# Optimization experiments

Measured on AMD Instinct MI355X. Metric: run time of the kernel, lower is better.

The kernel has to match this reference:

```python
import jax, jax.numpy as jnp
import numpy as np

EPS = 1e-7  # K.epsilon()

def squash(s, axis=-1):
    # v = (|s|^2 / (1+|s|^2)) * s / |s|
    sq_norm = jnp.sum(jnp.square(s), axis=axis, keepdims=True)
    return (sq_norm / (1.0 + sq_norm)) * s / jnp.sqrt(sq_norm + EPS)

def setup_inputs() -> dict:
    key = jax.random.key(0)
    k1, k2 = jax.random.split(key)
    B, IN_CAPS, IN_DIM = 256, 1152, 8
    NUM_CAPS, DIM_VEC = 10, 16
    inputs = jax.random.normal(k1, (B, IN_CAPS, IN_DIM), dtype=jnp.float32)
    W = jax.random.normal(k2, (IN_CAPS, NUM_CAPS, IN_DIM, DIM_VEC), dtype=jnp.float32) * 0.05
    bias = jnp.zeros((1, IN_CAPS, NUM_CAPS, 1), dtype=jnp.float32)
    return {"inputs": inputs, "W": W, "bias": bias}

def reference(inputs, W, bias):
    NUM_ROUTING = 3
    # tf.scan batch_dot -> one batched contraction over input_dim_vector
    # inputs: [b, i, d]; W: [i, c, d, v] -> u_hat: [b, i, c, v]
    u_hat = jnp.einsum('bid,icdv->bicv', inputs, W)
    b = bias  # [1, i, c, 1] routing logits
    for r in range(NUM_ROUTING):
        c = jax.nn.softmax(b, axis=2)                      # over num_capsule
        s = jnp.sum(c * u_hat, axis=1, keepdims=True)      # [b, 1, c, v]
        outputs = squash(s, axis=-1)
        if r != NUM_ROUTING - 1:
            # agreement: [b, i, c, 1]
            b = b + jnp.sum(u_hat * outputs, axis=-1, keepdims=True)
    B = inputs.shape[0]
    return jnp.reshape(outputs, (B, outputs.shape[2], outputs.shape[3]))
```

## Files before the change

### kernel.cpp

```cpp
#include <hip/hip_runtime.h>
#include <hip/hip_fp16.h>


#define N_I  1152
#define N_C  10
#define N_Bt 256
#define CV   160
#define NSPL 4
#define ISPL 288

__global__ __launch_bounds__(320) void k_uhat(const float* __restrict__ inp,
                                              const float* __restrict__ W,
                                              __half* __restrict__ uhat,
                                              int b_base, int sn) {
    const int i   = blockIdx.x;
    const int bl0 = blockIdx.y * 64;
    __shared__ float Wl[N_C * 132];
    {
        const int t4 = threadIdx.x * 4;
        const float4 w4 = *reinterpret_cast<const float4*>(W + (size_t)i * 1280 + t4);
        const int c = t4 >> 7, rem = t4 & 127;
        *reinterpret_cast<float4*>(&Wl[c * 132 + rem]) = w4;
    }
    __syncthreads();
    const int cv  = threadIdx.x % 40;
    const int bs0 = threadIdx.x / 40;
    const int c = cv >> 2, vq = cv & 3;
    const float* wbase = &Wl[c * 132 + vq * 4];
    float4 Wr[8];
    #pragma unroll
    for (int d = 0; d < 8; ++d) Wr[d] = *reinterpret_cast<const float4*>(wbase + d * 16);

    for (int s = 0; s < sn; ++s) {
        const int bo = bl0 + s * 8 + bs0;
        const float* ib = inp + ((size_t)(b_base + bo) * N_I + i) * 8;
        const float4 xa = *reinterpret_cast<const float4*>(ib);
        const float4 xb = *reinterpret_cast<const float4*>(ib + 4);
        float4 acc = {0.f, 0.f, 0.f, 0.f};
        acc.x = xa.x * Wr[0].x; acc.y = xa.x * Wr[0].y;
        acc.z = xa.x * Wr[0].z; acc.w = xa.x * Wr[0].w;
        acc.x += xa.y * Wr[1].x; acc.y += xa.y * Wr[1].y;
        acc.z += xa.y * Wr[1].z; acc.w += xa.y * Wr[1].w;
        acc.x += xa.z * Wr[2].x; acc.y += xa.z * Wr[2].y;
        acc.z += xa.z * Wr[2].z; acc.w += xa.z * Wr[2].w;
        acc.x += xa.w * Wr[3].x; acc.y += xa.w * Wr[3].y;
        acc.z += xa.w * Wr[3].z; acc.w += xa.w * Wr[3].w;
        acc.x += xb.x * Wr[4].x; acc.y += xb.x * Wr[4].y;
        acc.z += xb.x * Wr[4].z; acc.w += xb.x * Wr[4].w;
        acc.x += xb.y * Wr[5].x; acc.y += xb.y * Wr[5].y;
        acc.z += xb.y * Wr[5].z; acc.w += xb.y * Wr[5].w;
        acc.x += xb.z * Wr[6].x; acc.y += xb.z * Wr[6].y;
        acc.z += xb.z * Wr[6].z; acc.w += xb.z * Wr[6].w;
        acc.x += xb.w * Wr[7].x; acc.y += xb.w * Wr[7].y;
        acc.z += xb.w * Wr[7].z; acc.w += xb.w * Wr[7].w;
        union { __half2 h[2]; uint2 u; } pk;
        pk.h[0] = __floats2half2_rn(acc.x, acc.y);
        pk.h[1] = __floats2half2_rn(acc.z, acc.w);
        *reinterpret_cast<uint2*>(uhat + ((size_t)bo * N_I + i) * CV + cv * 4) = pk.u;
    }
}

template <int MODE>
__global__ __launch_bounds__(576) void k_route(const __half* __restrict__ uhat,
                                               const float* __restrict__ bias,
                                               const float* __restrict__ osum,
                                               float* __restrict__ s_part) {
    const int bl  = blockIdx.x >> 2;
    const int spl = blockIdx.x & 3;
    const int t  = threadIdx.x;
    const int vq = t & 3;
    const int ig = t >> 2;
    __shared__ float sred[9 * CV];

    float4 os[N_C];
    if constexpr (MODE) {
        const float* ob = osum + bl * CV;
        #pragma unroll
        for (int c = 0; c < N_C; ++c)
            os[c] = *reinterpret_cast<const float4*>(ob + c * 16 + vq * 4);
    }

    float4 sp[N_C];
    #pragma unroll
    for (int c = 0; c < N_C; ++c) sp[c] = {0.f, 0.f, 0.f, 0.f};

    #pragma unroll
    for (int ii = 0; ii < 2; ++ii) {
        const int i = spl * ISPL + ii * 144 + ig;
        const __half* up = uhat + ((size_t)bl * N_I + i) * CV + vq * 4;
        float4 u[N_C];
        #pragma unroll
        for (int c = 0; c < N_C; ++c) {
            union { uint2 u2; __half2 h[2]; } r;
            r.u2 = *reinterpret_cast<const uint2*>(up + c * 16);
            const float2 f0 = __half22float2(r.h[0]);
            const float2 f1 = __half22float2(r.h[1]);
            u[c] = {f0.x, f0.y, f1.x, f1.y};
        }
        float lg[N_C];
        #pragma unroll
        for (int c = 0; c < N_C; ++c) {
            float dd = 0.f;
            if constexpr (MODE) {
                dd = u[c].x * os[c].x + u[c].y * os[c].y +
                     u[c].z * os[c].z + u[c].w * os[c].w;
                dd += __shfl_xor(dd, 1);
                dd += __shfl_xor(dd, 2);
            }
            lg[c] = dd + bias[i * N_C + c];
        }
        float m = lg[0];
        #pragma unroll
        for (int c = 1; c < N_C; ++c) m = fmaxf(m, lg[c]);
        float ssum = 0.f;
        #pragma unroll
        for (int c = 0; c < N_C; ++c) { lg[c] = __expf(lg[c] - m); ssum += lg[c]; }
        const float inv = 1.0f / ssum;
        #pragma unroll
        for (int c = 0; c < N_C; ++c) {
            const float wc = lg[c] * inv;
            sp[c].x += wc * u[c].x;
            sp[c].y += wc * u[c].y;
            sp[c].z += wc * u[c].z;
            sp[c].w += wc * u[c].w;
        }
    }

    #pragma unroll
    for (int c = 0; c < N_C; ++c) {
        #pragma unroll
        for (int off = 4; off <= 32; off <<= 1) {
            sp[c].x += __shfl_xor(sp[c].x, off);
            sp[c].y += __shfl_xor(sp[c].y, off);
            sp[c].z += __shfl_xor(sp[c].z, off);
            sp[c].w += __shfl_xor(sp[c].w, off);
        }
    }
    const int lane = t & 63, wv = t >> 6;
    if (lane < 4) {
        #pragma unroll
        for (int c = 0; c < N_C; ++c)
            *reinterpret_cast<float4*>(&sred[wv * CV + lane * 40 + c * 4]) = sp[c];
    }
    __syncthreads();
    if (t < CV) {
        const int cc = t >> 4, v = t & 15, vq2 = v >> 2, j = v & 3;
        float s = 0.f;
        #pragma unroll
        for (int w = 0; w < 9; ++w) s += sred[w * CV + vq2 * 40 + cc * 4 + j];
        s_part[((size_t)bl * NSPL + spl) * CV + t] = s;
    }
}

template <int OM>
__global__ __launch_bounds__(160) void k_squash(const float* __restrict__ s_part,
                                                const float* __restrict__ osum_in,
                                                float* __restrict__ dst, int b_off) {
    const int bl = blockIdx.x;
    const int t  = threadIdx.x;
    float s = 0.f;
    #pragma unroll
    for (int k = 0; k < NSPL; ++k) s += s_part[((size_t)bl * NSPL + k) * CV + t];
    float sq = s * s;
    sq += __shfl_xor(sq, 1);
    sq += __shfl_xor(sq, 2);
    sq += __shfl_xor(sq, 4);
    sq += __shfl_xor(sq, 8);
    const float o = s * (sq / (1.0f + sq)) / sqrtf(sq + 1e-7f);
    if constexpr (OM == 1)      dst[bl * CV + t] = osum_in[bl * CV + t] + o;
    else if constexpr (OM == 2) dst[((size_t)(b_off + bl)) * CV + t] = o;
    else                        dst[bl * CV + t] = o;
}

extern "C" void kernel_launch(void* const* d_in, const int* in_sizes, int n_in,
                              void* d_out, int out_size, void* d_ws, size_t ws_size,
                              hipStream_t stream) {
    (void)in_sizes; (void)n_in; (void)out_size;
    const float* inp  = (const float*)d_in[0];
    const float* W    = (const float*)d_in[1];
    const float* bias = (const float*)d_in[2];
    float* out = (float*)d_out;

    int bn = 256;
    while (bn > 32) {
        size_t need = (size_t)bn * N_I * CV * 2
                    + (size_t)bn * NSPL * CV * 4
                    + 2ull * bn * CV * 4;
        if (need <= ws_size) break;
        bn >>= 1;
    }

    __half* uhat  = (__half*)d_ws;
    float* s_part = (float*)((char*)d_ws + (size_t)bn * N_I * CV * 2);
    float* osum_a = s_part + (size_t)bn * NSPL * CV;
    float* osum_b = osum_a + (size_t)bn * CV;

    const int sn = (bn < 64 ? bn : 64) >> 3;
    const dim3 gu(N_I, (unsigned)((bn + 63) / 64));

    for (int b0 = 0; b0 < N_Bt; b0 += bn) {
        k_uhat<<<gu, 320, 0, stream>>>(inp, W, uhat, b0, sn);
        k_route<0><<<bn * NSPL, 576, 0, stream>>>(uhat, bias, nullptr, s_part);
        k_squash<0><<<bn, 160, 0, stream>>>(s_part, nullptr, osum_a, 0);
        k_route<1><<<bn * NSPL, 576, 0, stream>>>(uhat, bias, osum_a, s_part);
        k_squash<1><<<bn, 160, 0, stream>>>(s_part, osum_a, osum_b, 0);
        k_route<1><<<bn * NSPL, 576, 0, stream>>>(uhat, bias, osum_b, s_part);
        k_squash<2><<<bn, 160, 0, stream>>>(s_part, nullptr, out, b0);
    }
}
```

Baseline: 193.3 us.

## Fuse squash into routing kernel with one 1024-thread block per batch

Each routing pass now runs one 1024-thread block per batch element that covers all input capsules, so the partial sums are reduced in shared memory and the squash is applied in place. This removes the separate squash kernels and the s_part round trip through global memory. Bias and the previous output are staged in shared memory first. The cost is a 46KB bias copy per block and fewer, larger blocks (256 instead of 1024), which may lower occupancy; the last of the five loop iterations is partly masked.

```diff
diff --git a/kernel.cpp b/kernel.cpp
--- a/kernel.cpp
+++ b/kernel.cpp
@@ -6,8 +6,6 @@
 #define N_C  10
 #define N_Bt 256
 #define CV   160
-#define NSPL 4
-#define ISPL 288
 
 __global__ __launch_bounds__(320) void k_uhat(const float* __restrict__ inp,
                                               const float* __restrict__ W,
@@ -36,23 +34,15 @@
         const float* ib = inp + ((size_t)(b_base + bo) * N_I + i) * 8;
         const float4 xa = *reinterpret_cast<const float4*>(ib);
         const float4 xb = *reinterpret_cast<const float4*>(ib + 4);
+        const float xs[8] = {xa.x, xa.y, xa.z, xa.w, xb.x, xb.y, xb.z, xb.w};
         float4 acc = {0.f, 0.f, 0.f, 0.f};
-        acc.x = xa.x * Wr[0].x; acc.y = xa.x * Wr[0].y;
-        acc.z = xa.x * Wr[0].z; acc.w = xa.x * Wr[0].w;
-        acc.x += xa.y * Wr[1].x; acc.y += xa.y * Wr[1].y;
-        acc.z += xa.y * Wr[1].z; acc.w += xa.y * Wr[1].w;
-        acc.x += xa.z * Wr[2].x; acc.y += xa.z * Wr[2].y;
-        acc.z += xa.z * Wr[2].z; acc.w += xa.z * Wr[2].w;
-        acc.x += xa.w * Wr[3].x; acc.y += xa.w * Wr[3].y;
-        acc.z += xa.w * Wr[3].z; acc.w += xa.w * Wr[3].w;
-        acc.x += xb.x * Wr[4].x; acc.y += xb.x * Wr[4].y;
-        acc.z += xb.x * Wr[4].z; acc.w += xb.x * Wr[4].w;
-        acc.x += xb.y * Wr[5].x; acc.y += xb.y * Wr[5].y;
-        acc.z += xb.y * Wr[5].z; acc.w += xb.y * Wr[5].w;
-        acc.x += xb.z * Wr[6].x; acc.y += xb.z * Wr[6].y;
-        acc.z += xb.z * Wr[6].z; acc.w += xb.z * Wr[6].w;
-        acc.x += xb.w * Wr[7].x; acc.y += xb.w * Wr[7].y;
-        acc.z += xb.w * Wr[7].z; acc.w += xb.w * Wr[7].w;
+        #pragma unroll
+        for (int d = 0; d < 8; ++d) {
+            acc.x += xs[d] * Wr[d].x;
+            acc.y += xs[d] * Wr[d].y;
+            acc.z += xs[d] * Wr[d].z;
+            acc.w += xs[d] * Wr[d].w;
+        }
         union { __half2 h[2]; uint2 u; } pk;
         pk.h[0] = __floats2half2_rn(acc.x, acc.y);
         pk.h[1] = __floats2half2_rn(acc.z, acc.w);
@@ -61,33 +51,42 @@
 }
 
 template <int MODE>
-__global__ __launch_bounds__(576) void k_route(const __half* __restrict__ uhat,
-                                               const float* __restrict__ bias,
-                                               const float* __restrict__ osum,
-                                               float* __restrict__ s_part) {
-    const int bl  = blockIdx.x >> 2;
-    const int spl = blockIdx.x & 3;
+__global__ __launch_bounds__(1024) void k_route(const __half* __restrict__ uhat,
+                                                const float* __restrict__ bias,
+                                                const float* __restrict__ osum_in,
+                                                float* __restrict__ dst,
+                                                int b_off) {
+    const int bl = blockIdx.x;
     const int t  = threadIdx.x;
     const int vq = t & 3;
     const int ig = t >> 2;
-    __shared__ float sred[9 * CV];
 
-    float4 os[N_C];
-    if constexpr (MODE) {
-        const float* ob = osum + bl * CV;
-        #pragma unroll
-        for (int c = 0; c < N_C; ++c)
-            os[c] = *reinterpret_cast<const float4*>(ob + c * 16 + vq * 4);
+    __shared__ float biasl[N_I * N_C];
+    __shared__ float osl[CV];
+    __shared__ float sred[16 * CV];
+
+    for (int j = t; j < N_I * N_C / 4; j += 1024)
+        reinterpret_cast<float4*>(biasl)[j] = reinterpret_cast<const float4*>(bias)[j];
+    if constexpr (MODE >= 1) {
+        if (t < 40)
+            reinterpret_cast<float4*>(osl)[t] =
+                reinterpret_cast<const float4*>(osum_in + bl * CV)[t];
     }
+    __syncthreads();
 
     float4 sp[N_C];
     #pragma unroll
     for (int c = 0; c < N_C; ++c) sp[c] = {0.f, 0.f, 0.f, 0.f};
 
+    const __half* ub = uhat + (size_t)bl * N_I * CV;
+
     #pragma unroll
-    for (int ii = 0; ii < 2; ++ii) {
-        const int i = spl * ISPL + ii * 144 + ig;
-        const __half* up = uhat + ((size_t)bl * N_I + i) * CV + vq * 4;
+    for (int k = 0; k < 5; ++k) {
+        const int ii = k * 256 + ig;
+        const bool ok = (ii < N_I);
+        const int i = ok ? ii : 0;
+        const __half* up = ub + (size_t)i * CV + vq * 4;
+
         float4 u[N_C];
         #pragma unroll
         for (int c = 0; c < N_C; ++c) {
@@ -97,17 +96,18 @@
             const float2 f1 = __half22float2(r.h[1]);
             u[c] = {f0.x, f0.y, f1.x, f1.y};
         }
+
         float lg[N_C];
         #pragma unroll
         for (int c = 0; c < N_C; ++c) {
             float dd = 0.f;
-            if constexpr (MODE) {
-                dd = u[c].x * os[c].x + u[c].y * os[c].y +
-                     u[c].z * os[c].z + u[c].w * os[c].w;
+            if constexpr (MODE >= 1) {
+                const float4 o4 = *reinterpret_cast<const float4*>(&osl[c * 16 + vq * 4]);
+                dd = u[c].x * o4.x + u[c].y * o4.y + u[c].z * o4.z + u[c].w * o4.w;
                 dd += __shfl_xor(dd, 1);
                 dd += __shfl_xor(dd, 2);
             }
-            lg[c] = dd + bias[i * N_C + c];
+            lg[c] = dd + biasl[i * N_C + c];
         }
         float m = lg[0];
         #pragma unroll
@@ -115,7 +115,8 @@
         float ssum = 0.f;
         #pragma unroll
         for (int c = 0; c < N_C; ++c) { lg[c] = __expf(lg[c] - m); ssum += lg[c]; }
-        const float inv = 1.0f / ssum;
+        float inv = 1.0f / ssum;
+        if (!ok) inv = 0.0f;
         #pragma unroll
         for (int c = 0; c < N_C; ++c) {
             const float wc = lg[c] * inv;
@@ -140,36 +141,24 @@
     if (lane < 4) {
         #pragma unroll
         for (int c = 0; c < N_C; ++c)
-            *reinterpret_cast<float4*>(&sred[wv * CV + lane * 40 + c * 4]) = sp[c];
+            *reinterpret_cast<float4*>(&sred[wv * CV + c * 16 + lane * 4]) = sp[c];
     }
     __syncthreads();
+
     if (t < CV) {
-        const int cc = t >> 4, v = t & 15, vq2 = v >> 2, j = v & 3;
         float s = 0.f;
         #pragma unroll
-        for (int w = 0; w < 9; ++w) s += sred[w * CV + vq2 * 40 + cc * 4 + j];
-        s_part[((size_t)bl * NSPL + spl) * CV + t] = s;
+        for (int w = 0; w < 16; ++w) s += sred[w * CV + t];
+        float sq = s * s;
+        sq += __shfl_xor(sq, 1);
+        sq += __shfl_xor(sq, 2);
+        sq += __shfl_xor(sq, 4);
+        sq += __shfl_xor(sq, 8);
+        const float o = s * (sq / (1.0f + sq)) / sqrtf(sq + 1e-7f);
+        if constexpr (MODE == 0)      dst[bl * CV + t] = o;
+        else if constexpr (MODE == 1) dst[bl * CV + t] = osl[t] + o;
+        else                          dst[((size_t)(b_off + bl)) * CV + t] = o;
     }
-}
-
-template <int OM>
-__global__ __launch_bounds__(160) void k_squash(const float* __restrict__ s_part,
-                                                const float* __restrict__ osum_in,
-                                                float* __restrict__ dst, int b_off) {
-    const int bl = blockIdx.x;
-    const int t  = threadIdx.x;
-    float s = 0.f;
-    #pragma unroll
-    for (int k = 0; k < NSPL; ++k) s += s_part[((size_t)bl * NSPL + k) * CV + t];
-    float sq = s * s;
-    sq += __shfl_xor(sq, 1);
-    sq += __shfl_xor(sq, 2);
-    sq += __shfl_xor(sq, 4);
-    sq += __shfl_xor(sq, 8);
-    const float o = s * (sq / (1.0f + sq)) / sqrtf(sq + 1e-7f);
-    if constexpr (OM == 1)      dst[bl * CV + t] = osum_in[bl * CV + t] + o;
-    else if constexpr (OM == 2) dst[((size_t)(b_off + bl)) * CV + t] = o;
-    else                        dst[bl * CV + t] = o;
 }
 
 extern "C" void kernel_launch(void* const* d_in, const int* in_sizes, int n_in,
@@ -184,15 +173,13 @@
     int bn = 256;
     while (bn > 32) {
         size_t need = (size_t)bn * N_I * CV * 2
-                    + (size_t)bn * NSPL * CV * 4
                     + 2ull * bn * CV * 4;
         if (need <= ws_size) break;
         bn >>= 1;
     }
 
     __half* uhat  = (__half*)d_ws;
-    float* s_part = (float*)((char*)d_ws + (size_t)bn * N_I * CV * 2);
-    float* osum_a = s_part + (size_t)bn * NSPL * CV;
+    float* osum_a = (float*)((char*)d_ws + (size_t)bn * N_I * CV * 2);
     float* osum_b = osum_a + (size_t)bn * CV;
 
     const int sn = (bn < 64 ? bn : 64) >> 3;
@@ -200,11 +187,8 @@
 
     for (int b0 = 0; b0 < N_Bt; b0 += bn) {
         k_uhat<<<gu, 320, 0, stream>>>(inp, W, uhat, b0, sn);
-        k_route<0><<<bn * NSPL, 576, 0, stream>>>(uhat, bias, nullptr, s_part);
-        k_squash<0><<<bn, 160, 0, stream>>>(s_part, nullptr, osum_a, 0);
-        k_route<1><<<bn * NSPL, 576, 0, stream>>>(uhat, bias, osum_a, s_part);
-        k_squash<1><<<bn, 160, 0, stream>>>(s_part, osum_a, osum_b, 0);
-        k_route<1><<<bn * NSPL, 576, 0, stream>>>(uhat, bias, osum_b, s_part);
-        k_squash<2><<<bn, 160, 0, stream>>>(s_part, nullptr, out, b0);
+        k_route<0><<<bn, 1024, 0, stream>>>(uhat, bias, nullptr, osum_a, 0);
+        k_route<1><<<bn, 1024, 0, stream>>>(uhat, bias, osum_a, osum_b, 0);
+        k_route<2><<<bn, 1024, 0, stream>>>(uhat, bias, osum_b, out, b0);
     }
 }
```

After: 323.7 us. 1.67x slower.
